# Kernel tuning notes

Measured on AMD Instinct MI355X. Metric: run time of the kernel, lower is better.

Reference implementation:

```python
import jax, jax.numpy as jnp
import numpy as np

C = 512
NUM_HEADS = 8
NUM_GROUPS = 32
EPS = 1e-5


def group_norm(x, w, b):
    # x: [B, C, H, W]
    B, Cc, H, W = x.shape
    xg = x.reshape(B, NUM_GROUPS, Cc // NUM_GROUPS, H, W)
    mu = jnp.mean(xg, axis=(2, 3, 4), keepdims=True)
    var = jnp.var(xg, axis=(2, 3, 4), keepdims=True)
    xn = ((xg - mu) * jax.lax.rsqrt(var + EPS)).reshape(B, Cc, H, W)
    return xn * w[None, :, None, None] + b[None, :, None, None]


def setup_inputs() -> dict:
    key = jax.random.key(0)
    ks = jax.random.split(key, 10)
    s = 1.0 / np.sqrt(C)
    x = jax.random.normal(ks[0], (16, C, 32, 32), dtype=jnp.float32)
    return {
        "x": x,
        "gn_w": jnp.ones((C,), jnp.float32),
        "gn_b": jnp.zeros((C,), jnp.float32),
        "wq": jax.random.uniform(ks[1], (C, C), jnp.float32, -s, s),
        "bq": jax.random.uniform(ks[2], (C,), jnp.float32, -s, s),
        "wk": jax.random.uniform(ks[3], (C, C), jnp.float32, -s, s),
        "bk": jax.random.uniform(ks[4], (C,), jnp.float32, -s, s),
        "wv": jax.random.uniform(ks[5], (C, C), jnp.float32, -s, s),
        "bv": jax.random.uniform(ks[6], (C,), jnp.float32, -s, s),
        "wo": jax.random.uniform(ks[7], (C, C), jnp.float32, -s, s),
    }


def reference(x, gn_w, gn_b, wq, bq, wk, bk, wv, bv, wo):
    B, Cc, H, W = x.shape
    dh = Cc // NUM_HEADS
    out = group_norm(x, gn_w, gn_b)
    # NCHW -> [B, HW, C]
    t = out.transpose(0, 2, 3, 1).reshape(B, H * W, Cc)
    # torch Linear: y = t @ W.T + b
    q = t @ wq.T + bq
    k = t @ wk.T + bk
    v = t @ wv.T + bv
    qh = q.reshape(B, H * W, NUM_HEADS, dh)
    kh = k.reshape(B, H * W, NUM_HEADS, dh)
    vh = v.reshape(B, H * W, NUM_HEADS, dh)
    # NOTE: original scales by full channel ** 0.5 (not per-head dim)
    score = jnp.einsum('bihc,bjhc->bijh', qh, kh) * (Cc ** -0.5)
    score = jax.nn.softmax(score, axis=2)
    attn = jnp.einsum('bijh,bjhc->bihc', score, vh).reshape(B, H * W, Cc)
    attn = attn @ wo.T  # no bias
    attn = attn.reshape(B, H, W, Cc).transpose(0, 3, 1, 2)
    return attn + x
```

## Files before the change

kernel.cpp:

```cpp
#include <hip/hip_runtime.h>
#include <hip/hip_bf16.h>
#include <stdint.h>

typedef __bf16 bf16x8 __attribute__((ext_vector_type(8)));
typedef float  f32x4  __attribute__((ext_vector_type(4)));
typedef float  f32x16 __attribute__((ext_vector_type(16)));
typedef unsigned short u16x8 __attribute__((ext_vector_type(8)));
typedef unsigned short u16x4 __attribute__((ext_vector_type(4)));
typedef unsigned int   u32x4_t __attribute__((ext_vector_type(4)));

#define MFMA16(a,b,c) __builtin_amdgcn_mfma_f32_16x16x32_bf16((a),(b),(c),0,0,0)
#define MFMA32(a,b,c) __builtin_amdgcn_mfma_f32_32x32x16_bf16((a),(b),(c),0,0,0)

#if __has_builtin(__builtin_amdgcn_exp2f)
#define EXP2F(x) __builtin_amdgcn_exp2f(x)
#else
#define EXP2F(x) exp2f(x)
#endif

static __device__ __forceinline__ unsigned short f2bf(float f) {
    __bf16 h = (__bf16)f;
    return __builtin_bit_cast(unsigned short, h);
}
static __device__ __forceinline__ unsigned pk2(float a, float b) {
    unsigned lo = (unsigned)__builtin_bit_cast(unsigned short, (__bf16)a);
    unsigned hi = (unsigned)__builtin_bit_cast(unsigned short, (__bf16)b);
    return lo | (hi << 16);
}
static __device__ __forceinline__ void swap32(unsigned &a, unsigned &b, const bool hib) {
    unsigned ax = (unsigned)__shfl_xor((int)a, 32, 64);
    unsigned bx = (unsigned)__shfl_xor((int)b, 32, 64);
    unsigned na = hib ? bx : a;
    unsigned nb = hib ? b  : ax;
    a = na; b = nb;
}

#define GL2LDS(g, l) __builtin_amdgcn_global_load_lds( \
    (const __attribute__((address_space(1))) void*)(const void*)(g), \
    (__attribute__((address_space(3))) void*)(void*)(l), 16, 0, 0)

__global__ __launch_bounds__(256) void wcvt_kernel(
    const float* __restrict__ wq, const float* __restrict__ wk,
    const float* __restrict__ wv, const float* __restrict__ wo,
    unsigned short* __restrict__ dst)
{
    int i = blockIdx.x * 256 + threadIdx.x;
    const float* srcs[4] = {wq, wk, wv, wo};
    int a   = i >> 14;
    int off = (i & 16383) * 16;
    const float* s = srcs[a] + off;
    unsigned short* d = dst + a * 262144 + off;
    #pragma unroll
    for (int p = 0; p < 4; ++p) {
        float4 f = *reinterpret_cast<const float4*>(s + p * 4);
        u16x4 o;
        o[0] = f2bf(f.x); o[1] = f2bf(f.y); o[2] = f2bf(f.z); o[3] = f2bf(f.w);
        *reinterpret_cast<u16x4*>(d + p * 4) = o;
    }
}

__global__ __launch_bounds__(256) void gn_kernel(
    const float* __restrict__ x, const float* __restrict__ gw,
    const float* __restrict__ gb, unsigned short* __restrict__ tb)
{
    const int tid = threadIdx.x;
    const int b = blockIdx.x >> 5;
    const int g = blockIdx.x & 31;
    const float* base = x + (size_t)(b * 512 + g * 16) * 1024;

    float4 v[16];
    float s1 = 0.f, s2 = 0.f;
    #pragma unroll
    for (int j = 0; j < 16; ++j) {
        v[j] = *reinterpret_cast<const float4*>(base + j * 1024 + tid * 4);
        s1 += v[j].x + v[j].y + v[j].z + v[j].w;
        s2 += v[j].x * v[j].x + v[j].y * v[j].y + v[j].z * v[j].z + v[j].w * v[j].w;
    }
    #pragma unroll
    for (int off = 32; off > 0; off >>= 1) {
        s1 += __shfl_xor(s1, off, 64);
        s2 += __shfl_xor(s2, off, 64);
    }
    __shared__ float red[8];
    __shared__ unsigned short ldsT[16 * 1024];
    const int wid = tid >> 6, lane = tid & 63;
    if (lane == 0) { red[wid] = s1; red[wid + 4] = s2; }
    __syncthreads();
    float S1 = red[0] + red[1] + red[2] + red[3];
    float S2 = red[4] + red[5] + red[6] + red[7];
    const float mean = S1 * (1.f / 16384.f);
    const float rstd = rsqrtf(S2 * (1.f / 16384.f) - mean * mean + 1e-5f);

    #pragma unroll
    for (int j = 0; j < 16; ++j) {
        const float ga = gw[g * 16 + j] * rstd;
        const float be = gb[g * 16 + j] - mean * ga;
        u16x4 o4;
        o4[0] = f2bf(v[j].x * ga + be);
        o4[1] = f2bf(v[j].y * ga + be);
        o4[2] = f2bf(v[j].z * ga + be);
        o4[3] = f2bf(v[j].w * ga + be);
        *reinterpret_cast<u16x4*>(&ldsT[j * 1024 + tid * 4]) = o4;
    }
    __syncthreads();
    #pragma unroll
    for (int r = 0; r < 4; ++r) {
        int hw = r * 256 + tid;
        u16x8 a, c;
        #pragma unroll
        for (int j = 0; j < 8; ++j) a[j] = ldsT[j * 1024 + hw];
        #pragma unroll
        for (int j = 0; j < 8; ++j) c[j] = ldsT[(8 + j) * 1024 + hw];
        size_t o = (size_t)(b * 1024 + hw) * 512 + g * 16;
        *reinterpret_cast<u16x8*>(tb + o)     = a;
        *reinterpret_cast<u16x8*>(tb + o + 8) = c;
    }
}

__global__ __launch_bounds__(256) void qkv_kernel(
    const unsigned short* __restrict__ tb, const unsigned short* __restrict__ wbf,
    const float* __restrict__ bq, const float* __restrict__ bk,
    const float* __restrict__ bv,
    unsigned short* __restrict__ qb, unsigned short* __restrict__ kb,
    unsigned short* __restrict__ vb)
{
    const int tid = threadIdx.x;
    const int m0 = blockIdx.x * 128;
    const int n0 = blockIdx.y * 128;
    const int z  = blockIdx.z;
    const unsigned short* W = wbf + z * 262144;
    const float* bias = (z == 0) ? bq : (z == 1) ? bk : bv;

    __shared__ unsigned short As[128 * 32];
    __shared__ unsigned short Bs[128 * 32];
    const int wid = tid >> 6, lane = tid & 63;
    const int lr = lane & 15, lg = lane >> 4;
    const int wr = wid >> 1, wc = wid & 1;
    const int row0 = tid >> 2, c16 = tid & 3;

    f32x4 acc[4][4] = {};
    for (int k0 = 0; k0 < 512; k0 += 32) {
        u16x8 ra0 = *reinterpret_cast<const u16x8*>(tb + (size_t)(m0 + row0) * 512 + k0 + c16 * 8);
        u16x8 ra1 = *reinterpret_cast<const u16x8*>(tb + (size_t)(m0 + row0 + 64) * 512 + k0 + c16 * 8);
        u16x8 rb0 = *reinterpret_cast<const u16x8*>(W + (size_t)(n0 + row0) * 512 + k0 + c16 * 8);
        u16x8 rb1 = *reinterpret_cast<const u16x8*>(W + (size_t)(n0 + row0 + 64) * 512 + k0 + c16 * 8);
        __syncthreads();
        *reinterpret_cast<u16x8*>(&As[tid * 8])         = ra0;
        *reinterpret_cast<u16x8*>(&As[(256 + tid) * 8]) = ra1;
        *reinterpret_cast<u16x8*>(&Bs[tid * 8])         = rb0;
        *reinterpret_cast<u16x8*>(&Bs[(256 + tid) * 8]) = rb1;
        __syncthreads();
        bf16x8 af[4], bfg[4];
        #pragma unroll
        for (int i = 0; i < 4; ++i) {
            af[i]  = *reinterpret_cast<const bf16x8*>(&As[(wr * 64 + i * 16 + lr) * 32 + lg * 8]);
            bfg[i] = *reinterpret_cast<const bf16x8*>(&Bs[(wc * 64 + i * 16 + lr) * 32 + lg * 8]);
        }
        #pragma unroll
        for (int i = 0; i < 4; ++i)
            #pragma unroll
            for (int j = 0; j < 4; ++j)
                acc[i][j] = MFMA16(af[i], bfg[j], acc[i][j]);
    }

    const float scale = (z == 0) ? 0.06375871598720551f : 1.0f;
    unsigned short* outp = (z == 0) ? qb : (z == 1) ? kb : vb;
    float bias4[4];
    #pragma unroll
    for (int j = 0; j < 4; ++j) bias4[j] = bias[n0 + wc * 64 + j * 16 + lr];

    if (z < 2) {
        #pragma unroll
        for (int i = 0; i < 4; ++i) {
            int mrow = m0 + wr * 64 + i * 16 + lg * 4;
            #pragma unroll
            for (int j = 0; j < 4; ++j) {
                int n = n0 + wc * 64 + j * 16 + lr;
                #pragma unroll
                for (int r = 0; r < 4; ++r)
                    outp[(size_t)(mrow + r) * 512 + n] = f2bf((acc[i][j][r] + bias4[j]) * scale);
            }
        }
    } else {
        #pragma unroll
        for (int i = 0; i < 4; ++i) {
            int mrow = m0 + wr * 64 + i * 16 + lg * 4;
            int bb = mrow >> 10, hw = mrow & 1023;
            #pragma unroll
            for (int j = 0; j < 4; ++j) {
                int n = n0 + wc * 64 + j * 16 + lr;
                u16x4 pk;
                #pragma unroll
                for (int r = 0; r < 4; ++r) pk[r] = f2bf(acc[i][j][r] + bias4[j]);
                *reinterpret_cast<u16x4*>(outp + (size_t)(bb * 512 + n) * 1024 + hw) = pk;
            }
        }
    }
}

__global__ __launch_bounds__(256, 4) void attn_kernel(
    const unsigned short* __restrict__ qb, const unsigned short* __restrict__ kb,
    const unsigned short* __restrict__ vt, unsigned short* __restrict__ ob)
{
    __shared__ __align__(16) char smc[33280];
    const int tid = threadIdx.x;
    const int wid = tid >> 6, lane = tid & 63;
    const int rQ = lane & 31;
    const bool hib = lane >= 32;
    const int hi16 = hib ? 16 : 0;
    const int swzA = (rQ & 7) << 4;

    const int bid = blockIdx.x;
    const int qt = (bid >> 3) & 7;
    const int g_ = (bid & 7) | ((bid >> 6) << 3);
    const int h = g_ & 7;
    const int b = g_ >> 3;
    const int q0 = qt * 128 + wid * 32;

    bf16x8 aq[4];
    {
        const unsigned short* qp = qb + (size_t)(b * 1024 + q0 + rQ) * 512 + h * 64 + (hib ? 8 : 0);
        #pragma unroll
        for (int kk = 0; kk < 4; ++kk)
            aq[kk] = *reinterpret_cast<const bf16x8*>(qp + kk * 16);
    }

    const int sRow = tid >> 3;
    const int colE = ((tid & 7) ^ (sRow & 7)) << 3;
    const unsigned short* kg = kb + (size_t)(b * 1024 + sRow) * 512 + h * 64 + colE;
    const unsigned short* vg = vt + (size_t)(b * 512 + h * 64 + sRow) * 1024 + colE;

#define STAGE(KG, VG, CURB) do { \
        char* KL_ = smc + (CURB) * 8192; \
        char* VL_ = smc + 16384 + (CURB) * 8192; \
        GL2LDS((KG),             KL_ + tid * 16); \
        GL2LDS((KG) + 32 * 512,  KL_ + 4096 + tid * 16); \
        GL2LDS((VG),             VL_ + tid * 16); \
        GL2LDS((VG) + 32 * 1024, VL_ + 4096 + tid * 16); \
    } while (0)

    STAGE(kg, vg, 0);
    const unsigned short* kgr = kg + 64 * 512;
    const unsigned short* vgr = vg + 64;

    f32x16 o0 = {}, o1 = {};
    float lsum = 0.f;
    int cur = 0;
    __syncthreads();

    for (int t = 0; t < 16; ++t) {
        if (t < 15) {
            STAGE(kgr, vgr, cur ^ 1);
            kgr += 64 * 512;
            vgr += 64;
        }
        const char* KL = smc + cur * 8192;
        const char* VL = smc + 16384 + cur * 8192;
        #pragma unroll
        for (int g = 0; g < 2; ++g) {
            f32x16 s = {};
            #pragma unroll
            for (int kk = 0; kk < 4; ++kk) {
                bf16x8 kf = *reinterpret_cast<const bf16x8*>(
                    KL + g * 4096 + rQ * 128 + ((kk * 32 + hi16) ^ swzA));
                s = MFMA32(kf, aq[kk], s);
            }
            #pragma unroll
            for (int r = 0; r < 16; ++r) s[r] = EXP2F(s[r]);
            float p01 = (s[0] + s[1]) + (s[2] + s[3]);
            float p23 = (s[4] + s[5]) + (s[6] + s[7]);
            float p45 = (s[8] + s[9]) + (s[10] + s[11]);
            float p67 = (s[12] + s[13]) + (s[14] + s[15]);
            lsum += (p01 + p23) + (p45 + p67);
            unsigned w0 = pk2(s[0], s[1]),   w1 = pk2(s[2], s[3]);
            unsigned w2 = pk2(s[4], s[5]),   w3 = pk2(s[6], s[7]);
            unsigned w4 = pk2(s[8], s[9]),   w5 = pk2(s[10], s[11]);
            unsigned w6 = pk2(s[12], s[13]), w7 = pk2(s[14], s[15]);
            swap32(w0, w2, hib); swap32(w1, w3, hib);
            swap32(w4, w6, hib); swap32(w5, w7, hib);
            u32x4_t fa = {w0, w1, w2, w3};
            u32x4_t fb = {w4, w5, w6, w7};
            bf16x8 pf0 = __builtin_bit_cast(bf16x8, fa);
            bf16x8 pf1 = __builtin_bit_cast(bf16x8, fb);
            #pragma unroll
            for (int hf = 0; hf < 2; ++hf) {
                bf16x8 pf = hf ? pf1 : pf0;
                const int ks = g * 2 + hf;
                bf16x8 v0 = *reinterpret_cast<const bf16x8*>(
                    VL + rQ * 128 + ((ks * 32 + hi16) ^ swzA));
                bf16x8 v1 = *reinterpret_cast<const bf16x8*>(
                    VL + 4096 + rQ * 128 + ((ks * 32 + hi16) ^ swzA));
                o0 = MFMA32(pf, v0, o0);
                o1 = MFMA32(pf, v1, o1);
            }
        }
        __syncthreads();
        cur ^= 1;
    }
#undef STAGE

    lsum += __shfl_xor(lsum, 32, 64);
    const float inv = 1.0f / lsum;
    float* sb = (float*)(smc + 32768);
    if (lane < 32) sb[wid * 32 + rQ] = inv;
    asm volatile("s_waitcnt lgkmcnt(0)" ::: "memory");
    float rinv[16];
    #pragma unroll
    for (int rg = 0; rg < 16; ++rg)
        rinv[rg] = sb[wid * 32 + ((rg & 3) + 8 * (rg >> 2) + (hib ? 4 : 0))];
    unsigned short* op = ob + (size_t)(b * 1024 + q0) * 512 + h * 64 + rQ;
    #pragma unroll
    for (int rg = 0; rg < 16; ++rg) {
        const int r = (rg & 3) + 8 * (rg >> 2) + (hib ? 4 : 0);
        op[(size_t)r * 512]      = f2bf(o0[rg] * rinv[rg]);
        op[(size_t)r * 512 + 32] = f2bf(o1[rg] * rinv[rg]);
    }
}

__global__ __launch_bounds__(256) void proj_kernel(
    const unsigned short* __restrict__ ab, const unsigned short* __restrict__ wobf,
    const float* __restrict__ x, float* __restrict__ out)
{
    const int tid = threadIdx.x;
    const int m0 = blockIdx.x * 128;
    const int n0 = blockIdx.y * 128;
    __shared__ unsigned short As[128 * 32];
    __shared__ unsigned short Bs[128 * 32];
    const int wid = tid >> 6, lane = tid & 63;
    const int lr = lane & 15, lg = lane >> 4;
    const int wr = wid >> 1, wc = wid & 1;
    const int row0 = tid >> 2, c16 = tid & 3;

    f32x4 acc[4][4] = {};
    for (int k0 = 0; k0 < 512; k0 += 32) {
        u16x8 ra0 = *reinterpret_cast<const u16x8*>(ab + (size_t)(m0 + row0) * 512 + k0 + c16 * 8);
        u16x8 ra1 = *reinterpret_cast<const u16x8*>(ab + (size_t)(m0 + row0 + 64) * 512 + k0 + c16 * 8);
        u16x8 rb0 = *reinterpret_cast<const u16x8*>(wobf + (size_t)(n0 + row0) * 512 + k0 + c16 * 8);
        u16x8 rb1 = *reinterpret_cast<const u16x8*>(wobf + (size_t)(n0 + row0 + 64) * 512 + k0 + c16 * 8);
        __syncthreads();
        *reinterpret_cast<u16x8*>(&As[tid * 8])         = ra0;
        *reinterpret_cast<u16x8*>(&As[(256 + tid) * 8]) = ra1;
        *reinterpret_cast<u16x8*>(&Bs[tid * 8])         = rb0;
        *reinterpret_cast<u16x8*>(&Bs[(256 + tid) * 8]) = rb1;
        __syncthreads();
        bf16x8 af[4], bfg[4];
        #pragma unroll
        for (int i = 0; i < 4; ++i) {
            af[i]  = *reinterpret_cast<const bf16x8*>(&As[(wr * 64 + i * 16 + lr) * 32 + lg * 8]);
            bfg[i] = *reinterpret_cast<const bf16x8*>(&Bs[(wc * 64 + i * 16 + lr) * 32 + lg * 8]);
        }
        #pragma unroll
        for (int i = 0; i < 4; ++i)
            #pragma unroll
            for (int j = 0; j < 4; ++j)
                acc[i][j] = MFMA16(af[i], bfg[j], acc[i][j]);
    }
    #pragma unroll
    for (int i = 0; i < 4; ++i) {
        int mrow = m0 + wr * 64 + i * 16 + lg * 4;
        int bb = mrow >> 10, hw = mrow & 1023;
        #pragma unroll
        for (int j = 0; j < 4; ++j) {
            int n = n0 + wc * 64 + j * 16 + lr;
            size_t oadr = (size_t)(bb * 512 + n) * 1024 + hw;
            float4 xr = *reinterpret_cast<const float4*>(x + oadr);
            float4 ov;
            ov.x = acc[i][j][0] + xr.x;
            ov.y = acc[i][j][1] + xr.y;
            ov.z = acc[i][j][2] + xr.z;
            ov.w = acc[i][j][3] + xr.w;
            *reinterpret_cast<float4*>(out + oadr) = ov;
        }
    }
}

extern "C" void kernel_launch(void* const* d_in, const int* in_sizes, int n_in,
                              void* d_out, int out_size, void* d_ws, size_t ws_size,
                              hipStream_t stream)
{
    const float* x  = (const float*)d_in[0];
    const float* gw = (const float*)d_in[1];
    const float* gb = (const float*)d_in[2];
    const float* wq = (const float*)d_in[3];
    const float* bq = (const float*)d_in[4];
    const float* wk = (const float*)d_in[5];
    const float* bk = (const float*)d_in[6];
    const float* wv = (const float*)d_in[7];
    const float* bv = (const float*)d_in[8];
    const float* wo = (const float*)d_in[9];
    float* out = (float*)d_out;

    char* ws = (char*)d_ws;
    unsigned short* wbf  = (unsigned short*)ws;
    unsigned short* tbuf = (unsigned short*)(ws + (2u  << 20));
    unsigned short* qbuf = (unsigned short*)(ws + (18u << 20));
    unsigned short* kbuf = (unsigned short*)(ws + (34u << 20));
    unsigned short* vbuf = (unsigned short*)(ws + (50u << 20));

    hipLaunchKernelGGL(wcvt_kernel, dim3(256), dim3(256), 0, stream, wq, wk, wv, wo, wbf);
    hipLaunchKernelGGL(gn_kernel, dim3(512), dim3(256), 0, stream, x, gw, gb, tbuf);
    hipLaunchKernelGGL(qkv_kernel, dim3(128, 4, 3), dim3(256), 0, stream,
                       tbuf, wbf, bq, bk, bv, qbuf, kbuf, vbuf);
    hipLaunchKernelGGL(attn_kernel, dim3(1024), dim3(256), 0, stream,
                       qbuf, kbuf, vbuf, tbuf);
    hipLaunchKernelGGL(proj_kernel, dim3(128, 4), dim3(256), 0, stream,
                       tbuf, wbf + 3 * 262144, x, out);
}
```

Baseline: 212.6 us.

## Use permlane32 swap, MFMA row-sum, and direct global-to-LDS loads in GEMMs

The attention kernel replaces the shuffle-based half-wave swap with the v_permlane32_swap instruction. It also replaces the scalar row-sum plus LDS broadcast of the softmax denominator with an extra MFMA against a vector of ones, which yields the sums directly in the output layout. The QKV and output-projection GEMMs switch from register-staged global loads to global_load_lds. The trade-off is one extra MFMA per PV step and bf16-rounded probabilities in the denominator. The GEMMs still synchronise right after issuing the loads, so the direct-to-LDS path gives no real prefetch overlap.

```diff
diff --git a/kernel.cpp b/kernel.cpp
--- a/kernel.cpp
+++ b/kernel.cpp
@@ -27,12 +27,8 @@
     unsigned hi = (unsigned)__builtin_bit_cast(unsigned short, (__bf16)b);
     return lo | (hi << 16);
 }
-static __device__ __forceinline__ void swap32(unsigned &a, unsigned &b, const bool hib) {
-    unsigned ax = (unsigned)__shfl_xor((int)a, 32, 64);
-    unsigned bx = (unsigned)__shfl_xor((int)b, 32, 64);
-    unsigned na = hib ? bx : a;
-    unsigned nb = hib ? b  : ax;
-    a = na; b = nb;
+static __device__ __forceinline__ void swap32(unsigned &a, unsigned &b) {
+    asm("v_permlane32_swap_b32 %0, %1" : "+v"(a), "+v"(b));
 }
 
 #define GL2LDS(g, l) __builtin_amdgcn_global_load_lds( \
@@ -140,15 +136,11 @@
 
     f32x4 acc[4][4] = {};
     for (int k0 = 0; k0 < 512; k0 += 32) {
-        u16x8 ra0 = *reinterpret_cast<const u16x8*>(tb + (size_t)(m0 + row0) * 512 + k0 + c16 * 8);
-        u16x8 ra1 = *reinterpret_cast<const u16x8*>(tb + (size_t)(m0 + row0 + 64) * 512 + k0 + c16 * 8);
-        u16x8 rb0 = *reinterpret_cast<const u16x8*>(W + (size_t)(n0 + row0) * 512 + k0 + c16 * 8);
-        u16x8 rb1 = *reinterpret_cast<const u16x8*>(W + (size_t)(n0 + row0 + 64) * 512 + k0 + c16 * 8);
-        __syncthreads();
-        *reinterpret_cast<u16x8*>(&As[tid * 8])         = ra0;
-        *reinterpret_cast<u16x8*>(&As[(256 + tid) * 8]) = ra1;
-        *reinterpret_cast<u16x8*>(&Bs[tid * 8])         = rb0;
-        *reinterpret_cast<u16x8*>(&Bs[(256 + tid) * 8]) = rb1;
+        __syncthreads();
+        GL2LDS(tb + (size_t)(m0 + row0) * 512 + k0 + c16 * 8,      &As[tid * 8]);
+        GL2LDS(tb + (size_t)(m0 + row0 + 64) * 512 + k0 + c16 * 8, &As[(256 + tid) * 8]);
+        GL2LDS(W  + (size_t)(n0 + row0) * 512 + k0 + c16 * 8,      &Bs[tid * 8]);
+        GL2LDS(W  + (size_t)(n0 + row0 + 64) * 512 + k0 + c16 * 8, &Bs[(256 + tid) * 8]);
         __syncthreads();
         bf16x8 af[4], bfg[4];
         #pragma unroll
@@ -202,7 +194,7 @@
     const unsigned short* __restrict__ qb, const unsigned short* __restrict__ kb,
     const unsigned short* __restrict__ vt, unsigned short* __restrict__ ob)
 {
-    __shared__ __align__(16) char smc[33280];
+    __shared__ __align__(16) char smc[32768];
     const int tid = threadIdx.x;
     const int wid = tid >> 6, lane = tid & 63;
     const int rQ = lane & 31;
@@ -224,6 +216,9 @@
         for (int kk = 0; kk < 4; ++kk)
             aq[kk] = *reinterpret_cast<const bf16x8*>(qp + kk * 16);
     }
+    bf16x8 vones;
+    #pragma unroll
+    for (int j = 0; j < 8; ++j) vones[j] = (__bf16)1.0f;
 
     const int sRow = tid >> 3;
     const int colE = ((tid & 7) ^ (sRow & 7)) << 3;
@@ -243,8 +238,7 @@
     const unsigned short* kgr = kg + 64 * 512;
     const unsigned short* vgr = vg + 64;
 
-    f32x16 o0 = {}, o1 = {};
-    float lsum = 0.f;
+    f32x16 o0 = {}, o1 = {}, osum = {};
     int cur = 0;
     __syncthreads();
 
@@ -267,17 +261,12 @@
             }
             #pragma unroll
             for (int r = 0; r < 16; ++r) s[r] = EXP2F(s[r]);
-            float p01 = (s[0] + s[1]) + (s[2] + s[3]);
-            float p23 = (s[4] + s[5]) + (s[6] + s[7]);
-            float p45 = (s[8] + s[9]) + (s[10] + s[11]);
-            float p67 = (s[12] + s[13]) + (s[14] + s[15]);
-            lsum += (p01 + p23) + (p45 + p67);
             unsigned w0 = pk2(s[0], s[1]),   w1 = pk2(s[2], s[3]);
             unsigned w2 = pk2(s[4], s[5]),   w3 = pk2(s[6], s[7]);
             unsigned w4 = pk2(s[8], s[9]),   w5 = pk2(s[10], s[11]);
             unsigned w6 = pk2(s[12], s[13]), w7 = pk2(s[14], s[15]);
-            swap32(w0, w2, hib); swap32(w1, w3, hib);
-            swap32(w4, w6, hib); swap32(w5, w7, hib);
+            swap32(w0, w2); swap32(w1, w3);
+            swap32(w4, w6); swap32(w5, w7);
             u32x4_t fa = {w0, w1, w2, w3};
             u32x4_t fb = {w4, w5, w6, w7};
             bf16x8 pf0 = __builtin_bit_cast(bf16x8, fa);
@@ -290,8 +279,9 @@
                     VL + rQ * 128 + ((ks * 32 + hi16) ^ swzA));
                 bf16x8 v1 = *reinterpret_cast<const bf16x8*>(
                     VL + 4096 + rQ * 128 + ((ks * 32 + hi16) ^ swzA));
-                o0 = MFMA32(pf, v0, o0);
-                o1 = MFMA32(pf, v1, o1);
+                o0   = MFMA32(pf, v0, o0);
+                o1   = MFMA32(pf, v1, o1);
+                osum = MFMA32(pf, vones, osum);
             }
         }
         __syncthreads();
@@ -299,21 +289,13 @@
     }
 #undef STAGE
 
-    lsum += __shfl_xor(lsum, 32, 64);
-    const float inv = 1.0f / lsum;
-    float* sb = (float*)(smc + 32768);
-    if (lane < 32) sb[wid * 32 + rQ] = inv;
-    asm volatile("s_waitcnt lgkmcnt(0)" ::: "memory");
-    float rinv[16];
-    #pragma unroll
-    for (int rg = 0; rg < 16; ++rg)
-        rinv[rg] = sb[wid * 32 + ((rg & 3) + 8 * (rg >> 2) + (hib ? 4 : 0))];
     unsigned short* op = ob + (size_t)(b * 1024 + q0) * 512 + h * 64 + rQ;
     #pragma unroll
     for (int rg = 0; rg < 16; ++rg) {
+        const float inv = 1.0f / osum[rg];
         const int r = (rg & 3) + 8 * (rg >> 2) + (hib ? 4 : 0);
-        op[(size_t)r * 512]      = f2bf(o0[rg] * rinv[rg]);
-        op[(size_t)r * 512 + 32] = f2bf(o1[rg] * rinv[rg]);
+        op[(size_t)r * 512]      = f2bf(o0[rg] * inv);
+        op[(size_t)r * 512 + 32] = f2bf(o1[rg] * inv);
     }
 }
 
@@ -333,15 +315,11 @@
 
     f32x4 acc[4][4] = {};
     for (int k0 = 0; k0 < 512; k0 += 32) {
-        u16x8 ra0 = *reinterpret_cast<const u16x8*>(ab + (size_t)(m0 + row0) * 512 + k0 + c16 * 8);
-        u16x8 ra1 = *reinterpret_cast<const u16x8*>(ab + (size_t)(m0 + row0 + 64) * 512 + k0 + c16 * 8);
-        u16x8 rb0 = *reinterpret_cast<const u16x8*>(wobf + (size_t)(n0 + row0) * 512 + k0 + c16 * 8);
-        u16x8 rb1 = *reinterpret_cast<const u16x8*>(wobf + (size_t)(n0 + row0 + 64) * 512 + k0 + c16 * 8);
-        __syncthreads();
-        *reinterpret_cast<u16x8*>(&As[tid * 8])         = ra0;
-        *reinterpret_cast<u16x8*>(&As[(256 + tid) * 8]) = ra1;
-        *reinterpret_cast<u16x8*>(&Bs[tid * 8])         = rb0;
-        *reinterpret_cast<u16x8*>(&Bs[(256 + tid) * 8]) = rb1;
+        __syncthreads();
+        GL2LDS(ab   + (size_t)(m0 + row0) * 512 + k0 + c16 * 8,      &As[tid * 8]);
+        GL2LDS(ab   + (size_t)(m0 + row0 + 64) * 512 + k0 + c16 * 8, &As[(256 + tid) * 8]);
+        GL2LDS(wobf + (size_t)(n0 + row0) * 512 + k0 + c16 * 8,      &Bs[tid * 8]);
+        GL2LDS(wobf + (size_t)(n0 + row0 + 64) * 512 + k0 + c16 * 8, &Bs[(256 + tid) * 8]);
         __syncthreads();
         bf16x8 af[4], bfg[4];
         #pragma unroll
```

Result: no change. 215.7 us (+1.5%).
